# Kernel optimization log

Measured on AMD Instinct MI355X. Metric: run time of the kernel, lower is better.

## Reference

```python
import jax, jax.numpy as jnp
import numpy as np

N, D = 2048, 64


def setup_inputs() -> dict:
    key = jax.random.key(0)
    y_samples = jax.random.normal(key, (N, D), dtype=jnp.float32)
    return {"y_samples": y_samples}


def reference(y_samples) -> jnp.ndarray:
    # mi_est_org (CLUB upper bound, non-variational):
    #   positive = 0
    #   negative[i, d] = -mean_j (y[j, d] - y[i, d])^2 / 2
    #   upper_bound = mean_i ( 0 - sum_d negative[i, d] )
    # prediction_1 = y[:, None, :]  (i axis), y_samples_1 = y[None, :, :] (j axis)
    diff = y_samples[None, :, :] - y_samples[:, None, :]          # [i=N, j=N, D]
    negative = -jnp.mean(diff * diff, axis=1) / 2.0               # mean over j -> [N, D]
    upper_bound = jnp.mean(-jnp.sum(negative, axis=-1))           # scalar
    return upper_bound
```

## Files before the change

### kernel.cpp

```cpp
#include <hip/hip_runtime.h>


#define N_ROWS 2048
#define D_COLS 64
#define BLOCKS_A 64
#define THREADS_A 256
#define ROWS_PER_BLOCK (N_ROWS / BLOCKS_A)

__global__ __launch_bounds__(THREADS_A)
void mi_partial_sums(const float* __restrict__ y, float* __restrict__ ws) {
    __shared__ float s1s[THREADS_A];
    __shared__ float s2s[THREADS_A];
    const int t    = threadIdx.x;
    const int col  = t & 63;
    const int rsub = t >> 6;
    const int rowBase = blockIdx.x * ROWS_PER_BLOCK;

    float s1 = 0.0f, s2 = 0.0f;
    #pragma unroll
    for (int k = 0; k < ROWS_PER_BLOCK / 4; ++k) {
        const int row = rowBase + rsub + k * 4;
        const float v = y[row * D_COLS + col];
        s1 += v;
        s2 += v * v;
    }
    s1s[t] = s1;
    s2s[t] = s2;
    __syncthreads();

    if (t < 64) {
        const float a1 = s1s[t] + s1s[t + 64] + s1s[t + 128] + s1s[t + 192];
        const float a2 = s2s[t] + s2s[t + 64] + s2s[t + 128] + s2s[t + 192];
        ws[blockIdx.x * 128 + t]      = a1;
        ws[blockIdx.x * 128 + 64 + t] = a2;
    }
}

__global__ __launch_bounds__(64)
void mi_finalize(const float* __restrict__ ws, float* __restrict__ out) {
    const int d = threadIdx.x;
    float S1 = 0.0f, S2 = 0.0f;
    #pragma unroll
    for (int b = 0; b < BLOCKS_A; ++b) {
        S1 += ws[b * 128 + d];
        S2 += ws[b * 128 + 64 + d];
    }
    const float invN = 1.0f / (float)N_ROWS;
    float v = S2 * invN - (S1 * invN) * (S1 * invN);

    #pragma unroll
    for (int off = 32; off > 0; off >>= 1)
        v += __shfl_down(v, off);

    if (d == 0) out[0] = v;
}

extern "C" void kernel_launch(void* const* d_in, const int* in_sizes, int n_in,
                              void* d_out, int out_size, void* d_ws, size_t ws_size,
                              hipStream_t stream) {
    const float* y = (const float*)d_in[0];
    float* out = (float*)d_out;
    float* ws  = (float*)d_ws;

    mi_partial_sums<<<BLOCKS_A, THREADS_A, 0, stream>>>(y, ws);
    mi_finalize<<<1, 64, 0, stream>>>(ws, out);
}
```

Before: 11.52 us.

## Fuse partial-sum and finalize kernels using per-block release flags

Merges the two launches into one kernel. Each block publishes its partial sums and sets a magic flag with a release store, and block 0 spin-waits on all 64 flags before reducing across 256 threads. This removes the second kernel launch and its inter-kernel gap. The cost is a spin-wait that depends on all 64 blocks being co-resident, and the flags are assumed to start without the magic value in the workspace.

```diff
diff --git a/kernel.cpp b/kernel.cpp
--- a/kernel.cpp
+++ b/kernel.cpp
@@ -3,24 +3,29 @@
 
 #define N_ROWS 2048
 #define D_COLS 64
-#define BLOCKS_A 64
-#define THREADS_A 256
-#define ROWS_PER_BLOCK (N_ROWS / BLOCKS_A)
+#define NBLK 64
+#define NTHR 256
+#define ROWS_PER_BLOCK (N_ROWS / NBLK)
+#define FLAG_MAGIC 0x5AC0FFEE0DDBA11ULL
 
-__global__ __launch_bounds__(THREADS_A)
-void mi_partial_sums(const float* __restrict__ y, float* __restrict__ ws) {
-    __shared__ float s1s[THREADS_A];
-    __shared__ float s2s[THREADS_A];
+
+__global__ __launch_bounds__(NTHR)
+void mi_fused(const float* __restrict__ y, float* __restrict__ ws,
+              float* __restrict__ out) {
+    __shared__ float s1s[NTHR];
+    __shared__ float s2s[NTHR];
+    unsigned long long* flags = (unsigned long long*)(ws + NBLK * 128);
+
     const int t    = threadIdx.x;
+    const int b    = blockIdx.x;
     const int col  = t & 63;
     const int rsub = t >> 6;
-    const int rowBase = blockIdx.x * ROWS_PER_BLOCK;
+    const int rowBase = b * ROWS_PER_BLOCK;
 
     float s1 = 0.0f, s2 = 0.0f;
     #pragma unroll
     for (int k = 0; k < ROWS_PER_BLOCK / 4; ++k) {
-        const int row = rowBase + rsub + k * 4;
-        const float v = y[row * D_COLS + col];
+        const float v = y[(rowBase + rsub + 4 * k) * D_COLS + col];
         s1 += v;
         s2 += v * v;
     }
@@ -31,28 +36,47 @@
     if (t < 64) {
         const float a1 = s1s[t] + s1s[t + 64] + s1s[t + 128] + s1s[t + 192];
         const float a2 = s2s[t] + s2s[t + 64] + s2s[t + 128] + s2s[t + 192];
-        ws[blockIdx.x * 128 + t]      = a1;
-        ws[blockIdx.x * 128 + 64 + t] = a2;
+        ws[b * 128 + t]      = a1;
+        ws[b * 128 + 64 + t] = a2;
     }
-}
+    if (t == 0)
+        __hip_atomic_store(&flags[b], FLAG_MAGIC, __ATOMIC_RELEASE,
+                           __HIP_MEMORY_SCOPE_AGENT);
 
-__global__ __launch_bounds__(64)
-void mi_finalize(const float* __restrict__ ws, float* __restrict__ out) {
-    const int d = threadIdx.x;
+    if (b != 0) return;
+
+    if (t < 64) {
+        while (__hip_atomic_load(&flags[t], __ATOMIC_ACQUIRE,
+                                 __HIP_MEMORY_SCOPE_AGENT) != FLAG_MAGIC) { }
+        __hip_atomic_store(&flags[t], 0ULL, __ATOMIC_RELAXED,
+                           __HIP_MEMORY_SCOPE_AGENT);
+    }
+    __syncthreads();
+
+    const int grp = t >> 6;
     float S1 = 0.0f, S2 = 0.0f;
     #pragma unroll
-    for (int b = 0; b < BLOCKS_A; ++b) {
-        S1 += ws[b * 128 + d];
-        S2 += ws[b * 128 + 64 + d];
+    for (int k = 0; k < 16; ++k) {
+        const int bb = grp * 16 + k;
+        S1 += __hip_atomic_load(&ws[bb * 128 + col], __ATOMIC_RELAXED,
+                                __HIP_MEMORY_SCOPE_AGENT);
+        S2 += __hip_atomic_load(&ws[bb * 128 + 64 + col], __ATOMIC_RELAXED,
+                                __HIP_MEMORY_SCOPE_AGENT);
     }
-    const float invN = 1.0f / (float)N_ROWS;
-    float v = S2 * invN - (S1 * invN) * (S1 * invN);
+    s1s[t] = S1;
+    s2s[t] = S2;
+    __syncthreads();
 
-    #pragma unroll
-    for (int off = 32; off > 0; off >>= 1)
-        v += __shfl_down(v, off);
-
-    if (d == 0) out[0] = v;
+    if (t < 64) {
+        const float T1 = s1s[t] + s1s[t + 64] + s1s[t + 128] + s1s[t + 192];
+        const float T2 = s2s[t] + s2s[t + 64] + s2s[t + 128] + s2s[t + 192];
+        const float invN = 1.0f / (float)N_ROWS;
+        float v = T2 * invN - (T1 * invN) * (T1 * invN);
+        #pragma unroll
+        for (int off = 32; off > 0; off >>= 1)
+            v += __shfl_down(v, off);
+        if (t == 0) out[0] = v;
+    }
 }
 
 extern "C" void kernel_launch(void* const* d_in, const int* in_sizes, int n_in,
@@ -62,6 +86,5 @@
     float* out = (float*)d_out;
     float* ws  = (float*)d_ws;
 
-    mi_partial_sums<<<BLOCKS_A, THREADS_A, 0, stream>>>(y, ws);
-    mi_finalize<<<1, 64, 0, stream>>>(ws, out);
+    mi_fused<<<NBLK, NTHR, 0, stream>>>(y, ws, out);
 }
```

Measured after the change: 9.488 us. 1.21x faster.
